# Kernel tuning notes

Hardware: AMD Instinct MI355X
Metric: run time of the kernel (lower is better)

Reference implementation:

```python
import jax, jax.numpy as jnp
import numpy as np

B, Cin, Cout, K, H, W = 16, 32, 32, 3, 256, 256
EMB = 256  # layer_pos_embedding_size == condition_size == 256


def setup_inputs() -> dict:
    key = jax.random.key(0)
    ks = jax.random.split(key, 7)
    return {
        "x": jax.random.normal(ks[0], (B, Cin, H, W), jnp.float32),
        "condition": jax.random.normal(ks[1], (B, EMB), jnp.float32),
        "layer_pos_embedding": jax.random.normal(ks[2], (B, EMB), jnp.float32),
        # base conv weight, stored [Cin, Cout, K, K] as in the torch module
        "weights": jax.random.normal(ks[3], (Cin, Cout, K, K), jnp.float32) * 0.05,
        "bias": jax.random.normal(ks[4], (Cout,), jnp.float32) * 0.05,
        # weightAdapt: Linear(2*EMB -> Cin); biasAdapt: Linear(2*EMB -> Cout)
        "wa_w": jax.random.normal(ks[5], (Cin, 2 * EMB), jnp.float32) * 0.04,
        "wa_b": jnp.zeros((Cin,), jnp.float32),
        "ba_w": jax.random.normal(ks[6], (Cout, 2 * EMB), jnp.float32) * 0.04,
        "ba_b": jnp.zeros((Cout,), jnp.float32),
    }


def reference(x, condition, layer_pos_embedding, weights, bias, wa_w, wa_b, ba_w, ba_b):
    # i = cat([condition, layer_pos_embedding])  -> [B, 2*EMB]
    i = jnp.concatenate([condition, layer_pos_embedding], axis=-1)
    wadapt = i @ wa_w.T + wa_b   # [B, Cin]  per-sample input-channel modulation
    badapt = i @ ba_w.T + ba_b   # [B, Cout] per-sample bias modulation
    # per-sample OIHW kernel: (weights [Cin,Cout,K,K] * wadapt[b,Cin,1,1,1]) rearranged
    kern = jnp.einsum('iokl,bi->boikl', weights, wadapt)  # [B, Cout, Cin, K, K]

    def conv1(xi, ki):
        # xi: [Cin,H,W], ki: [Cout,Cin,K,K] -> [Cout,H,W], padding='same', stride 1
        return jax.lax.conv_general_dilated(
            xi[None], ki, window_strides=(1, 1), padding='SAME',
            dimension_numbers=('NCHW', 'OIHW', 'NCHW'))[0]

    o = jax.vmap(conv1)(x, kern)  # [B, Cout, H, W] (== groups=batch grouped conv)
    # modulated bias add per (batch, out_channel)
    return o + (bias[None, :] * badapt)[:, :, None, None]
```

## Files before the change

### kernel.cpp

```cpp
#include <hip/hip_runtime.h>


#define B_    16
#define CIN   32
#define COUT  32
#define H_    256
#define W_    256
#define EMB2  512

#define XPX   66
#define PXS   32
#define ROWS_ (XPX*PXS)
#define NSLOT 8

using short8  = __attribute__((ext_vector_type(8))) short;
using float4v = __attribute__((ext_vector_type(4))) float;
using float4r = __attribute__((ext_vector_type(4))) float;

__device__ __forceinline__ unsigned short f2bf(float f) {
    unsigned u = __builtin_bit_cast(unsigned, f);
    u += 0x7FFFu + ((u >> 16) & 1u);
    return (unsigned short)(u >> 16);
}
__device__ __forceinline__ unsigned pk2(float a, float b) {
    return (unsigned)f2bf(a) | ((unsigned)f2bf(b) << 16);
}

__global__ __launch_bounds__(256) void adapt_kernel(
    const float* __restrict__ cond, const float* __restrict__ lpe,
    const float* __restrict__ wa_w, const float* __restrict__ wa_b,
    const float* __restrict__ ba_w, const float* __restrict__ ba_b,
    const float* __restrict__ bias, float* __restrict__ ws)
{
    __shared__ float iv[EMB2];
    __shared__ float partial[64][4];
    const int b = blockIdx.x;
    const int t = threadIdx.x;

    iv[t]       = cond[b*256 + t];
    iv[t + 256] = lpe[b*256 + t];
    __syncthreads();

    const int out  = t & 63;
    const int part = t >> 6;
    const float* row = (out < 32) ? (wa_w + out*EMB2) : (ba_w + (out-32)*EMB2);
    float s = 0.f;
    #pragma unroll 8
    for (int j = part*128; j < part*128 + 128; ++j) s += iv[j] * row[j];
    partial[out][part] = s;
    __syncthreads();

    if (t < 64) {
        float v = partial[t][0] + partial[t][1] + partial[t][2] + partial[t][3];
        if (t < 32) ws[b*32 + t] = v + wa_b[t];
        else {
            int o = t - 32;
            ws[512 + b*32 + o] = bias[o] * (v + ba_b[o]);
        }
    }
}

__global__ __launch_bounds__(256, 3) void conv_kernel(
    const float* __restrict__ x, const float* __restrict__ weights,
    const float* __restrict__ ws, float* __restrict__ out)
{
    __shared__ __align__(16) unsigned short xbuf[NSLOT * ROWS_];
    __shared__ __align__(16) unsigned short wbuf[9 * 2 * 64 * 8];

    const int tid    = threadIdx.x;
    const int lane   = tid & 63;
    const int w      = tid >> 6;
    const int ln15   = lane & 15;
    const int kg     = lane >> 4;
    const int xstrip = blockIdx.x * 64;
    const int ystrip = blockIdx.y * 32;
    const int b      = blockIdx.z;

    for (int idx = tid; idx < CIN*COUT*9; idx += 256) {
        int i   = idx / 288;
        int rem = idx - i*288;
        int o   = rem / 9;
        int tap = rem - o*9;
        float v = weights[idx] * ws[b*32 + i];
        wbuf[((tap*2 + (o>>4))*64 + ((i>>3)*16 + (o&15)))*8 + (i&7)] = f2bf(v);
    }

    auto ld_main = [&](int gy, int g, int q, float4r (&L)[8]) {
        if ((unsigned)gy < 256u) {
            const float* src = x + (((size_t)(b*CIN + g*8) << 16) + (gy << 8)
                                    + (xstrip + 4*q));
            #pragma unroll
            for (int j = 0; j < 8; ++j)
                L[j] = *(const float4r*)&src[(size_t)j << 16];
        } else {
            #pragma unroll
            for (int j = 0; j < 8; ++j) L[j] = float4r{0.f, 0.f, 0.f, 0.f};
        }
    };
    auto wr_main = [&](int r, int g, int q, const float4r (&L)[8]) {
        unsigned slot = (unsigned)(r + 1) & 7;
        #pragma unroll
        for (int n = 0; n < 4; ++n) {
            int k = (n + q) & 3;
            int p = 4*q + k + 1;
            uint4 pk;
            pk.x = pk2(L[0][k], L[1][k]);
            pk.y = pk2(L[2][k], L[3][k]);
            pk.z = pk2(L[4][k], L[5][k]);
            pk.w = pk2(L[6][k], L[7][k]);
            *(uint4*)&xbuf[slot*ROWS_ + p*PXS + ((g ^ ((p >> 1) & 3)) * 8)] = pk;
        }
    };
    auto load8 = [&](int g, int yy, int xx, float (&f)[8]) {
        if (((unsigned)yy < 256u) & ((unsigned)xx < 256u)) {
            const float* src = x + (((size_t)(b*CIN + g*8) << 16) + (yy << 8) + xx);
            #pragma unroll
            for (int j = 0; j < 8; ++j) f[j] = src[(size_t)j << 16];
        } else {
            #pragma unroll
            for (int j = 0; j < 8; ++j) f[j] = 0.f;
        }
    };
    auto packwrite = [&](int r, int p, int g, const float (&f)[8]) {
        unsigned slot = (unsigned)(r + 1) & 7;
        unsigned dst  = slot*ROWS_ + p*PXS + ((g ^ ((p >> 1) & 3)) * 8);
        uint4 pk;
        pk.x = pk2(f[0], f[1]); pk.y = pk2(f[2], f[3]);
        pk.z = pk2(f[4], f[5]); pk.w = pk2(f[6], f[7]);
        *(uint4*)&xbuf[dst] = pk;
    };

    #pragma unroll
    for (int k2 = 0; k2 < 2; ++k2) {
        int ci = tid + k2*256;
        if (ci < 384) {
            int q = ci & 15, g = (ci >> 4) & 3, rr = ci >> 6;
            float4r L[8];
            ld_main(ystrip + rr - 1, g, q, L);
            wr_main(rr - 1, g, q, L);
        }
    }
    if (tid < 48) {
        int s = tid & 1, g = (tid >> 1) & 3, rr = tid >> 3;
        int p = s ? 65 : 0;
        float f[8];
        load8(g, ystrip + rr - 1, xstrip + p - 1, f);
        packwrite(rr - 1, p, g, f);
    }

    float bm[2][4];
    #pragma unroll
    for (int ot = 0; ot < 2; ++ot)
        #pragma unroll
        for (int r = 0; r < 4; ++r)
            bm[ot][r] = ws[512 + b*32 + ot*16 + kg*4 + r];

    float4r PM[8];
    float   PH[8];
    auto pf_issue = [&](int r0) {
        int q = tid & 15, g = (tid >> 4) & 3, rr = tid >> 6;
        ld_main(ystrip + r0 + rr, g, q, PM);
        if (tid < 32) {
            int s = tid & 1, hg = (tid >> 1) & 3, hr = tid >> 3;
            int p = s ? 65 : 0;
            load8(hg, ystrip + r0 + hr, xstrip + p - 1, PH);
        }
    };
    auto pf_write = [&](int r0) {
        int q = tid & 15, g = (tid >> 4) & 3, rr = tid >> 6;
        wr_main(r0 + rr, g, q, PM);
        if (tid < 32) {
            int s = tid & 1, hg = (tid >> 1) & 3, hr = tid >> 3;
            int p = s ? 65 : 0;
            packwrite(r0 + hr, p, hg, PH);
        }
    };

    pf_issue(5);

    asm volatile("s_waitcnt lgkmcnt(0)" ::: "memory");
    __builtin_amdgcn_s_barrier();
    asm volatile("" ::: "memory");

    for (int t = 0; t < 8; ++t) {
        const int orow = 4*t + w;
        const int gy   = ystrip + orow;

        float4v acc[4][2];
        #pragma unroll
        for (int c = 0; c < 4; ++c) {
            acc[c][0] = float4v{0.f, 0.f, 0.f, 0.f};
            acc[c][1] = float4v{0.f, 0.f, 0.f, 0.f};
        }

        #pragma unroll
        for (int dy = 0; dy < 3; ++dy) {
            const int rowbase = ((orow + dy) & 7) * ROWS_;
            #pragma unroll
            for (int dx = 0; dx < 3; ++dx) {
                const int tap = dy*3 + dx;
                short8 a0 = *(const short8*)&wbuf[((tap*2 + 0)*64 + lane)*8];
                short8 a1 = *(const short8*)&wbuf[((tap*2 + 1)*64 + lane)*8];
                #pragma unroll
                for (int c = 0; c < 4; ++c) {
                    int p = c*16 + dx + ln15;
                    int a = rowbase + p*PXS + ((kg ^ ((p >> 1) & 3)) * 8);
                    short8 xf = *(const short8*)&xbuf[a];
                    acc[c][0] = __builtin_amdgcn_mfma_f32_16x16x32_bf16(
                                    a0, xf, acc[c][0], 0, 0, 0);
                    acc[c][1] = __builtin_amdgcn_mfma_f32_16x16x32_bf16(
                                    a1, xf, acc[c][1], 0, 0, 0);
                }
            }
        }

        asm volatile("s_waitcnt lgkmcnt(0)" ::: "memory");
        __builtin_amdgcn_s_barrier();
        asm volatile("" ::: "memory");

        #pragma unroll
        for (int c = 0; c < 4; ++c) {
            const int xcol = xstrip + c*16 + ln15;
            #pragma unroll
            for (int ot = 0; ot < 2; ++ot) {
                const int obase = ot*16 + kg*4;
                #pragma unroll
                for (int r = 0; r < 4; ++r) {
                    out[((size_t)(b*COUT + obase + r)*256 + gy)*256 + xcol] =
                        acc[c][ot][r] + bm[ot][r];
                }
            }
        }

        if (t < 7) {
            pf_write(4*t + 5);
            if (t < 6) pf_issue(4*t + 9);
            asm volatile("s_waitcnt lgkmcnt(0)" ::: "memory");
            __builtin_amdgcn_s_barrier();
            asm volatile("" ::: "memory");
        }
    }
}

extern "C" void kernel_launch(void* const* d_in, const int* in_sizes, int n_in,
                              void* d_out, int out_size, void* d_ws, size_t ws_size,
                              hipStream_t stream) {
    const float* x       = (const float*)d_in[0];
    const float* cond    = (const float*)d_in[1];
    const float* lpe     = (const float*)d_in[2];
    const float* weights = (const float*)d_in[3];
    const float* bias    = (const float*)d_in[4];
    const float* wa_w    = (const float*)d_in[5];
    const float* wa_b    = (const float*)d_in[6];
    const float* ba_w    = (const float*)d_in[7];
    const float* ba_b    = (const float*)d_in[8];
    float* outp = (float*)d_out;
    float* ws   = (float*)d_ws;

    adapt_kernel<<<dim3(B_), dim3(256), 0, stream>>>(
        cond, lpe, wa_w, wa_b, ba_w, ba_b, bias, ws);

    conv_kernel<<<dim3(W_/64, H_/32, B_), dim3(256), 0, stream>>>(
        x, weights, ws, outp);
}
```

Before: 296.2 us.

## Give each wavefront private 3-row ring buffer and drop block barriers in conv loop

New measurement: 315.2 us. 1.06x slower.

```diff
diff --git a/kernel.cpp b/kernel.cpp
--- a/kernel.cpp
+++ b/kernel.cpp
@@ -11,7 +11,7 @@
 #define XPX   66
 #define PXS   32
 #define ROWS_ (XPX*PXS)
-#define NSLOT 8
+#define WSLOT 3
 
 using short8  = __attribute__((ext_vector_type(8))) short;
 using float4v = __attribute__((ext_vector_type(4))) float;
@@ -60,11 +60,11 @@
     }
 }
 
-__global__ __launch_bounds__(256, 3) void conv_kernel(
+__global__ __launch_bounds__(256, 2) void conv_kernel(
     const float* __restrict__ x, const float* __restrict__ weights,
     const float* __restrict__ ws, float* __restrict__ out)
 {
-    __shared__ __align__(16) unsigned short xbuf[NSLOT * ROWS_];
+    __shared__ __align__(16) unsigned short xbuf[4 * WSLOT * ROWS_];
     __shared__ __align__(16) unsigned short wbuf[9 * 2 * 64 * 8];
 
     const int tid    = threadIdx.x;
@@ -85,7 +85,10 @@
         wbuf[((tap*2 + (o>>4))*64 + ((i>>3)*16 + (o&15)))*8 + (i&7)] = f2bf(v);
     }
 
-    auto ld_main = [&](int gy, int g, int q, float4r (&L)[8]) {
+    const int q = lane & 15;
+    const int g = lane >> 4;
+
+    auto ld_main = [&](int gy, float4r (&L)[8]) {
         if ((unsigned)gy < 256u) {
             const float* src = x + (((size_t)(b*CIN + g*8) << 16) + (gy << 8)
                                     + (xstrip + 4*q));
@@ -97,8 +100,9 @@
             for (int j = 0; j < 8; ++j) L[j] = float4r{0.f, 0.f, 0.f, 0.f};
         }
     };
-    auto wr_main = [&](int r, int g, int q, const float4r (&L)[8]) {
-        unsigned slot = (unsigned)(r + 1) & 7;
+    auto wr_main = [&](int j, const float4r (&L)[8]) {
+        unsigned slot = (unsigned)(j + 1) % 3u;
+        unsigned base = (w*WSLOT + slot) * ROWS_;
         #pragma unroll
         for (int n = 0; n < 4; ++n) {
             int k = (n + q) & 3;
@@ -108,12 +112,14 @@
             pk.y = pk2(L[2][k], L[3][k]);
             pk.z = pk2(L[4][k], L[5][k]);
             pk.w = pk2(L[6][k], L[7][k]);
-            *(uint4*)&xbuf[slot*ROWS_ + p*PXS + ((g ^ ((p >> 1) & 3)) * 8)] = pk;
-        }
-    };
-    auto load8 = [&](int g, int yy, int xx, float (&f)[8]) {
-        if (((unsigned)yy < 256u) & ((unsigned)xx < 256u)) {
-            const float* src = x + (((size_t)(b*CIN + g*8) << 16) + (yy << 8) + xx);
+            *(uint4*)&xbuf[base + p*PXS + ((g ^ ((p >> 1) & 3)) * 8)] = pk;
+        }
+    };
+    auto ld_halo = [&](int gy, float (&f)[8]) {
+        int side = lane & 1, hg = (lane >> 1) & 3;
+        int xx = xstrip + (side ? 64 : -1);
+        if (((unsigned)gy < 256u) & ((unsigned)xx < 256u)) {
+            const float* src = x + (((size_t)(b*CIN + hg*8) << 16) + (gy << 8) + xx);
             #pragma unroll
             for (int j = 0; j < 8; ++j) f[j] = src[(size_t)j << 16];
         } else {
@@ -121,32 +127,16 @@
             for (int j = 0; j < 8; ++j) f[j] = 0.f;
         }
     };
-    auto packwrite = [&](int r, int p, int g, const float (&f)[8]) {
-        unsigned slot = (unsigned)(r + 1) & 7;
-        unsigned dst  = slot*ROWS_ + p*PXS + ((g ^ ((p >> 1) & 3)) * 8);
+    auto wr_halo = [&](int j, const float (&f)[8]) {
+        int side = lane & 1, hg = (lane >> 1) & 3;
+        int p = side ? 65 : 0;
+        unsigned slot = (unsigned)(j + 1) % 3u;
+        unsigned base = (w*WSLOT + slot) * ROWS_;
         uint4 pk;
         pk.x = pk2(f[0], f[1]); pk.y = pk2(f[2], f[3]);
         pk.z = pk2(f[4], f[5]); pk.w = pk2(f[6], f[7]);
-        *(uint4*)&xbuf[dst] = pk;
-    };
-
-    #pragma unroll
-    for (int k2 = 0; k2 < 2; ++k2) {
-        int ci = tid + k2*256;
-        if (ci < 384) {
-            int q = ci & 15, g = (ci >> 4) & 3, rr = ci >> 6;
-            float4r L[8];
-            ld_main(ystrip + rr - 1, g, q, L);
-            wr_main(rr - 1, g, q, L);
-        }
-    }
-    if (tid < 48) {
-        int s = tid & 1, g = (tid >> 1) & 3, rr = tid >> 3;
-        int p = s ? 65 : 0;
-        float f[8];
-        load8(g, ystrip + rr - 1, xstrip + p - 1, f);
-        packwrite(rr - 1, p, g, f);
-    }
+        *(uint4*)&xbuf[base + p*PXS + ((hg ^ ((p >> 1) & 3)) * 8)] = pk;
+    };
 
     float bm[2][4];
     #pragma unroll
@@ -155,36 +145,37 @@
         for (int r = 0; r < 4; ++r)
             bm[ot][r] = ws[512 + b*32 + ot*16 + kg*4 + r];
 
-    float4r PM[8];
-    float   PH[8];
-    auto pf_issue = [&](int r0) {
-        int q = tid & 15, g = (tid >> 4) & 3, rr = tid >> 6;
-        ld_main(ystrip + r0 + rr, g, q, PM);
-        if (tid < 32) {
-            int s = tid & 1, hg = (tid >> 1) & 3, hr = tid >> 3;
-            int p = s ? 65 : 0;
-            load8(hg, ystrip + r0 + hr, xstrip + p - 1, PH);
-        }
-    };
-    auto pf_write = [&](int r0) {
-        int q = tid & 15, g = (tid >> 4) & 3, rr = tid >> 6;
-        wr_main(r0 + rr, g, q, PM);
-        if (tid < 32) {
-            int s = tid & 1, hg = (tid >> 1) & 3, hr = tid >> 3;
-            int p = s ? 65 : 0;
-            packwrite(r0 + hr, p, hg, PH);
-        }
-    };
-
-    pf_issue(5);
-
-    asm volatile("s_waitcnt lgkmcnt(0)" ::: "memory");
-    __builtin_amdgcn_s_barrier();
-    asm volatile("" ::: "memory");
-
-    for (int t = 0; t < 8; ++t) {
-        const int orow = 4*t + w;
+    __syncthreads();
+
+    float4r La[8], Lb[8];
+    float   PHa[8], PHb[8];
+    {
+        ld_main(ystrip + 8*w - 1, La);
+        if (lane < 8) ld_halo(ystrip + 8*w - 1, PHa);
+        wr_main(8*w - 1, La);
+        if (lane < 8) wr_halo(8*w - 1, PHa);
+        ld_main(ystrip + 8*w, La);
+        if (lane < 8) ld_halo(ystrip + 8*w, PHa);
+        wr_main(8*w, La);
+        if (lane < 8) wr_halo(8*w, PHa);
+    }
+    ld_main(ystrip + 8*w + 1, La);
+    if (lane < 8) ld_halo(ystrip + 8*w + 1, PHa);
+
+    auto conv_iter = [&](int r, float4r (&LC)[8], float (&PHc)[8],
+                         float4r (&LN)[8], float (&PHn)[8], bool issue) {
+        const int orow = 8*w + r;
         const int gy   = ystrip + orow;
+
+        asm volatile("s_waitcnt lgkmcnt(0)" ::: "memory");
+        wr_main(orow + 1, LC);
+        if (lane < 8) wr_halo(orow + 1, PHc);
+        if (issue) {
+            ld_main(ystrip + orow + 2, LN);
+            if (lane < 8) ld_halo(ystrip + orow + 2, PHn);
+        }
+        asm volatile("s_waitcnt lgkmcnt(0)" ::: "memory");
+        asm volatile("" ::: "memory");
 
         float4v acc[4][2];
         #pragma unroll
@@ -195,7 +186,8 @@
 
         #pragma unroll
         for (int dy = 0; dy < 3; ++dy) {
-            const int rowbase = ((orow + dy) & 7) * ROWS_;
+            int s3 = (orow + dy) % 3;
+            const int rowbase = (w*WSLOT + s3) * ROWS_;
             #pragma unroll
             for (int dx = 0; dx < 3; ++dx) {
                 const int tap = dy*3 + dx;
@@ -214,10 +206,6 @@
             }
         }
 
-        asm volatile("s_waitcnt lgkmcnt(0)" ::: "memory");
-        __builtin_amdgcn_s_barrier();
-        asm volatile("" ::: "memory");
-
         #pragma unroll
         for (int c = 0; c < 4; ++c) {
             const int xcol = xstrip + c*16 + ln15;
@@ -225,20 +213,17 @@
             for (int ot = 0; ot < 2; ++ot) {
                 const int obase = ot*16 + kg*4;
                 #pragma unroll
-                for (int r = 0; r < 4; ++r) {
-                    out[((size_t)(b*COUT + obase + r)*256 + gy)*256 + xcol] =
-                        acc[c][ot][r] + bm[ot][r];
+                for (int r2 = 0; r2 < 4; ++r2) {
+                    out[((size_t)(b*COUT + obase + r2)*256 + gy)*256 + xcol] =
+                        acc[c][ot][r2] + bm[ot][r2];
                 }
             }
         }
-
-        if (t < 7) {
-            pf_write(4*t + 5);
-            if (t < 6) pf_issue(4*t + 9);
-            asm volatile("s_waitcnt lgkmcnt(0)" ::: "memory");
-            __builtin_amdgcn_s_barrier();
-            asm volatile("" ::: "memory");
-        }
+    };
+
+    for (int rr = 0; rr < 4; ++rr) {
+        conv_iter(2*rr,     La, PHa, Lb, PHb, true);
+        conv_iter(2*rr + 1, Lb, PHb, La, PHa, rr < 3);
     }
 }
 
```
